# Kernel tuning notes

Hardware: AMD Instinct MI355X
Metric: run time of the kernel (lower is better)

The kernel has to match this reference:

```python
import jax, jax.numpy as jnp
import numpy as np

N_NODES, N_EDGES, WIDTH = 50000, 640000, 128


def setup_inputs() -> dict:
    key = jax.random.key(0)
    k1, k2, k3 = jax.random.split(key, 3)
    x = jax.random.normal(k1, (N_NODES, WIDTH), dtype=jnp.float32)
    e = jax.random.randint(k2, (2, N_EDGES), 0, N_NODES, dtype=jnp.int32)
    # LinearBlock(2*width, width): Linear(256 -> 128) + ReLU
    W = jax.random.normal(k3, (WIDTH, 2 * WIDTH), dtype=jnp.float32) * (1.0 / np.sqrt(2 * WIDTH))
    b = jnp.zeros((WIDTH,), dtype=jnp.float32)
    return {"x": x, "e": e, "W": W, "b": b}


def reference(x, e, W, b):
    src, dst = e[0], e[1]
    # gather-subtract: diffs[k] = x[dst_k] - x[src_k]  -> [E, width]
    diffs = x[dst] - x[src]
    n = x.shape[0]
    # scatter_max over destination nodes; torch_scatter leaves empty segments at 0
    maxes = jax.ops.segment_max(diffs, dst, num_segments=n)  # [N, width]
    deg = jax.ops.segment_sum(jnp.ones((dst.shape[0],), jnp.float32), dst, num_segments=n)
    maxes = jnp.where((deg > 0)[:, None], maxes, 0.0)
    # LinearBlock (Linear + ReLU) on concat, then residual
    h = jnp.concatenate([x, maxes], axis=1)  # [N, 2*width]
    return x + jax.nn.relu(h @ W.T + b)
```

## Files before the change

### kernel.cpp

```cpp
#include <hip/hip_runtime.h>
#include <hip/hip_bf16.h>

#define WIDTH   128
#define NNODES  50000
#define NEDGES  640000
#define NTILES  3125
#define WLDS_STRIDE 264

#define RBLK    32
#define SSEG    8
#define RSZ     1563
#define SEG_I4  20000
#define C0      16
#define CAPB    128

#define BIN_BLOCKS  (RBLK * SSEG)
#define CVT_BLOCKS  1563
#define GRID_PREP   (BIN_BLOCKS + CVT_BLOCKS + 1)

typedef __attribute__((ext_vector_type(8))) short  short8;
typedef __attribute__((ext_vector_type(4))) short  short4_t;
typedef __attribute__((ext_vector_type(4))) float  float4_t;

__device__ inline short f2bf(float f) {
    union { float f; unsigned int u; } a;
    a.f = f;
    unsigned int r = a.u + 0x7FFFu + ((a.u >> 16) & 1u);
    return (short)(r >> 16);
}
__device__ inline unsigned int pack2bf(float a, float b) {
    unsigned int lo = (unsigned short)f2bf(a);
    unsigned int hi = (unsigned short)f2bf(b);
    return lo | (hi << 16);
}
__device__ inline float bflo(unsigned int u) { return __uint_as_float(u << 16); }
__device__ inline float bfhi(unsigned int u) { return __uint_as_float(u & 0xFFFF0000u); }

__global__ __launch_bounds__(1024) void prep_kernel(
    const float* __restrict__ x, const int* __restrict__ e,
    const float* __restrict__ W,
    uint2* __restrict__ xb2, uint2* __restrict__ wb2,
    int* __restrict__ counts2, int* __restrict__ buckets)
{
    __shared__ int cnt[RSZ];
    const int bid = blockIdx.x;
    const int tid = threadIdx.x;

    if (bid < BIN_BLOCKS) {
        int r = bid & (RBLK - 1);
        int s = bid >> 5;
        int base = r * RSZ;
        int rsz  = NNODES - base; if (rsz > RSZ) rsz = RSZ;

        for (int i = tid; i < RSZ; i += 1024) cnt[i] = 0;
        __syncthreads();

        const int4* dst4 = (const int4*)(e + NEDGES + s * (SEG_I4 * 4));
        const int4* src4 = (const int4*)(e + s * (SEG_I4 * 4));

        int i = tid;
        int4 d = (i < SEG_I4) ? dst4[i] : make_int4(-1, -1, -1, -1);
        while (i < SEG_I4) {
            int inx = i + 1024;
            int4 dn = d;
            if (inx < SEG_I4) dn = dst4[inx];

            unsigned a0 = (unsigned)(d.x - base);
            unsigned a1 = (unsigned)(d.y - base);
            unsigned a2 = (unsigned)(d.z - base);
            unsigned a3 = (unsigned)(d.w - base);
            bool m0 = a0 < (unsigned)rsz;
            bool m1 = a1 < (unsigned)rsz;
            bool m2 = a2 < (unsigned)rsz;
            bool m3 = a3 < (unsigned)rsz;
            if (m0 | m1 | m2 | m3) {
                int4 sv = src4[i];
                if (m0) { int p = atomicAdd(&cnt[a0], 1); if (p < C0) buckets[d.x * CAPB + s * C0 + p] = sv.x; }
                if (m1) { int p = atomicAdd(&cnt[a1], 1); if (p < C0) buckets[d.y * CAPB + s * C0 + p] = sv.y; }
                if (m2) { int p = atomicAdd(&cnt[a2], 1); if (p < C0) buckets[d.z * CAPB + s * C0 + p] = sv.z; }
                if (m3) { int p = atomicAdd(&cnt[a3], 1); if (p < C0) buckets[d.w * CAPB + s * C0 + p] = sv.w; }
            }
            d = dn; i = inx;
        }
        __syncthreads();
        for (int i2 = tid; i2 < rsz; i2 += 1024) {
            int c = cnt[i2]; if (c > C0) c = C0;
            counts2[(base + i2) * SSEG + s] = c;
        }
    } else if (bid < BIN_BLOCKS + CVT_BLOCKS) {
        int i = (bid - BIN_BLOCKS) * 1024 + tid;
        if (i < 1600000) {
            float4 v = ((const float4*)x)[i];
            uint2 p; p.x = pack2bf(v.x, v.y); p.y = pack2bf(v.z, v.w);
            xb2[i] = p;
        }
    } else {
        for (int j = tid; j < 8192; j += 1024) {
            float4 v = ((const float4*)W)[j];
            uint2 p; p.x = pack2bf(v.x, v.y); p.y = pack2bf(v.z, v.w);
            wb2[j] = p;
        }
    }
}

__global__ __launch_bounds__(256) void gather_min_bf16_kernel(
    const uint2* __restrict__ xb2, const int* __restrict__ counts2,
    const int* __restrict__ buckets, uint2* __restrict__ maxes2)
{
    int wave = (blockIdx.x * 256 + threadIdx.x) >> 6;
    int lane = threadIdx.x & 63;
    if (wave >= NNODES) return;
    int node = wave;

    int s0 = lane >> 4;
    int j  = lane & 15;
    int c0 = counts2[node * SSEG + s0];
    int c1 = counts2[node * SSEG + 4 + s0];
    int idx0 = buckets[node * CAPB + lane];
    int idx1 = buckets[node * CAPB + 64 + lane];
    bool v0 = j < c0;
    bool v1 = j < c1;
    unsigned long long m0 = __ballot(v0);
    unsigned long long m1 = __ballot(v1);
    int p0 = __builtin_amdgcn_mbcnt_hi((unsigned)(m0 >> 32),
             __builtin_amdgcn_mbcnt_lo((unsigned)m0, 0));
    int popc0 = __popcll(m0);
    int p1 = popc0 + __builtin_amdgcn_mbcnt_hi((unsigned)(m1 >> 32),
                     __builtin_amdgcn_mbcnt_lo((unsigned)m1, 0));
    int deg = popc0 + __popcll(m1);
    int t0 = v0 ? p0 : 63;
    int t1 = v1 ? p1 : 63;
    int r0 = __builtin_amdgcn_ds_permute(t0 << 2, idx0);
    int r1 = __builtin_amdgcn_ds_permute(t1 << 2, idx1);
    int myidx = (lane < popc0) ? r0 : r1;

    int h  = lane >> 5;
    int cl = lane & 31;

    float4 m; m.x = 3.4e38f; m.y = 3.4e38f; m.z = 3.4e38f; m.w = 3.4e38f;
#pragma unroll 1
    for (int j0 = 0; j0 < deg; j0 += 16) {
        uint2 v[8];
#pragma unroll
        for (int u = 0; u < 8; ++u) {
            int jc = j0 + 2 * u + h;
            jc = jc < deg ? jc : deg - 1;
            int src = __shfl(myidx, jc);
            v[u] = xb2[(size_t)src * 32 + cl];
        }
#pragma unroll
        for (int u = 0; u < 8; ++u) {
            m.x = fminf(m.x, bflo(v[u].x));
            m.y = fminf(m.y, bfhi(v[u].x));
            m.z = fminf(m.z, bflo(v[u].y));
            m.w = fminf(m.w, bfhi(v[u].y));
        }
    }
    m.x = fminf(m.x, __shfl_xor(m.x, 32));
    m.y = fminf(m.y, __shfl_xor(m.y, 32));
    m.z = fminf(m.z, __shfl_xor(m.z, 32));
    m.w = fminf(m.w, __shfl_xor(m.w, 32));

    if (h == 0) {
        uint2 o;
        if (deg > 0) {
            uint2 xv = xb2[(size_t)node * 32 + cl];
            o.x = pack2bf(bflo(xv.x) - m.x, bfhi(xv.x) - m.y);
            o.y = pack2bf(bflo(xv.y) - m.z, bfhi(xv.y) - m.w);
        } else {
            o.x = 0u; o.y = 0u;
        }
        maxes2[(size_t)node * 32 + cl] = o;
    }
}

__global__ __launch_bounds__(256) void fill_kernel(
    const int* __restrict__ e, int* __restrict__ counts, int* __restrict__ buckets)
{
    int i = blockIdx.x * 256 + threadIdx.x;
    if (i >= NEDGES) return;
    int src = e[i];
    int dst = e[NEDGES + i];
    int pos = atomicAdd(&counts[dst], 1);
    if (pos < 64) buckets[dst * 64 + pos] = src;
}

__global__ __launch_bounds__(256) void gather_min_fp32_kernel(
    const float* __restrict__ x, const int* __restrict__ counts,
    const int* __restrict__ buckets, unsigned int* __restrict__ maxes_u32)
{
    int wave = (blockIdx.x * 256 + threadIdx.x) >> 6;
    int lane = threadIdx.x & 63;
    if (wave >= NNODES) return;
    int node = wave;
    int deg  = counts[node];
    deg = deg > 64 ? 64 : deg;

    int myidx = (lane < deg) ? buckets[node * 64 + lane] : 0;
    int c = lane * 2;
    float2 m; m.x = 3.4e38f; m.y = 3.4e38f;
#pragma unroll 1
    for (int j0 = 0; j0 < deg; j0 += 8) {
        float2 v[8];
#pragma unroll
        for (int u = 0; u < 8; ++u) {
            int jc = j0 + u;
            jc = jc < deg ? jc : deg - 1;
            int src = __shfl(myidx, jc);
            v[u] = *(const float2*)(x + (size_t)src * WIDTH + c);
        }
#pragma unroll
        for (int u = 0; u < 8; ++u) {
            m.x = fminf(m.x, v[u].x);
            m.y = fminf(m.y, v[u].y);
        }
    }
    float2 o;
    if (deg > 0) {
        float2 xv = *(const float2*)(x + (size_t)node * WIDTH + c);
        o.x = xv.x - m.x;
        o.y = xv.y - m.y;
    } else { o.x = 0.f; o.y = 0.f; }
    maxes_u32[(size_t)node * 64 + lane] = pack2bf(o.x, o.y);
}

template<bool FAST>
__global__ __launch_bounds__(256, 2) void fused_gemm_kernel(
    const float* __restrict__ x, const short* __restrict__ xb,
    const short* __restrict__ maxes,
    const float* __restrict__ W, const short* __restrict__ Wb,
    const float* __restrict__ b, float* __restrict__ out)
{
    __shared__ short Wlds[WIDTH * WLDS_STRIDE];

    const int t = threadIdx.x;

    if (FAST) {
#pragma unroll
        for (int i = 0; i < 32; ++i) {
            int idx8 = t + i * 256;
            int flat = idx8 << 3;
            short8 w = *(const short8*)(Wb + flat);
            int n = flat >> 8;
            int k = flat & 255;
            *(short4_t*)&Wlds[n * WLDS_STRIDE + k]     = *(short4_t*)&w;
            *(short4_t*)&Wlds[n * WLDS_STRIDE + k + 4] = *((short4_t*)&w + 1);
        }
    } else {
#pragma unroll
        for (int i = 0; i < 32; ++i) {
            int idx4 = t + i * 256;
            int flat = idx4 << 2;
            float4 w = *(const float4*)(W + flat);
            int n = flat >> 8;
            int k = flat & 255;
            short4_t s;
            s.x = f2bf(w.x); s.y = f2bf(w.y); s.z = f2bf(w.z); s.w = f2bf(w.w);
            *(short4_t*)&Wlds[n * WLDS_STRIDE + k] = s;
        }
    }
    __syncthreads();

    const int wave  = t >> 6;
    const int lane  = t & 63;
    const int lm    = lane & 15;
    const int quad  = lane >> 4;
    const int nhalf = wave & 1;
    const int wpair = wave >> 1;
    const int ncol_base = nhalf * 64;

    short8 bfrag[4][8];
#pragma unroll
    for (int nt = 0; nt < 4; ++nt) {
        int n = ncol_base + nt * 16 + lm;
#pragma unroll
        for (int kt = 0; kt < 8; ++kt) {
            int k = kt * 32 + quad * 8;
            bfrag[nt][kt] = *(const short8*)&Wlds[n * WLDS_STRIDE + k];
        }
    }

    const int stride = gridDim.x * 2;
#pragma unroll 1
    for (int tile = blockIdx.x * 2 + wpair; tile < NTILES; tile += stride) {
        int row = tile * 16 + lm;
        const float* xr  = x     + (size_t)row * WIDTH;
        const short* xbr = FAST ? (xb + (size_t)row * WIDTH) : nullptr;
        const short* mr  = maxes + (size_t)row * WIDTH;

        float4_t acc[4];
#pragma unroll
        for (int nt = 0; nt < 4; ++nt) { acc[nt].x = 0.f; acc[nt].y = 0.f; acc[nt].z = 0.f; acc[nt].w = 0.f; }

#pragma unroll
        for (int kt = 0; kt < 8; ++kt) {
            int k = kt * 32 + quad * 8;
            short8 afrag;
            if (k < WIDTH) {
                if (FAST) {
                    afrag = *(const short8*)(xbr + k);
                } else {
                    float4 v0 = *(const float4*)(xr + k);
                    float4 v1 = *(const float4*)(xr + k + 4);
                    afrag[0] = f2bf(v0.x); afrag[1] = f2bf(v0.y);
                    afrag[2] = f2bf(v0.z); afrag[3] = f2bf(v0.w);
                    afrag[4] = f2bf(v1.x); afrag[5] = f2bf(v1.y);
                    afrag[6] = f2bf(v1.z); afrag[7] = f2bf(v1.w);
                }
            } else {
                afrag = *(const short8*)(mr + (k - WIDTH));
            }
#pragma unroll
            for (int nt = 0; nt < 4; ++nt) {
                acc[nt] = __builtin_amdgcn_mfma_f32_16x16x32_bf16(
                    afrag, bfrag[nt][kt], acc[nt], 0, 0, 0);
            }
        }

#pragma unroll
        for (int nt = 0; nt < 4; ++nt) {
            int col = ncol_base + nt * 16 + lm;
            float bias = b[col];
#pragma unroll
            for (int r = 0; r < 4; ++r) {
                int orow = tile * 16 + quad * 4 + r;
                float v = acc[nt][r] + bias;
                v = v > 0.f ? v : 0.f;
                size_t off = (size_t)orow * WIDTH + col;
                out[off] = x[off] + v;
            }
        }
    }
}

extern "C" void kernel_launch(void* const* d_in, const int* in_sizes, int n_in,
                              void* d_out, int out_size, void* d_ws, size_t ws_size,
                              hipStream_t stream) {
    const float* x = (const float*)d_in[0];
    const int*   e = (const int*)  d_in[1];
    const float* W = (const float*)d_in[2];
    const float* b = (const float*)d_in[3];
    float* out = (float*)d_out;

    char* ws = (char*)d_ws;

    const size_t off_buckets = 1600512;
    const size_t off_maxes   = off_buckets + 25600000;
    const size_t off_xb      = off_maxes + 12800000;
    const size_t off_wb      = off_xb + 12800000;
    const size_t need        = off_wb + 65536;

    if (ws_size >= need) {
        int*          counts2 = (int*)ws;
        int*          buckets = (int*)(ws + off_buckets);
        unsigned int* maxes   = (unsigned int*)(ws + off_maxes);
        short*        xb      = (short*)(ws + off_xb);
        short*        wb      = (short*)(ws + off_wb);

        prep_kernel<<<GRID_PREP, 1024, 0, stream>>>(
            x, e, W, (uint2*)xb, (uint2*)wb, counts2, buckets);
        gather_min_bf16_kernel<<<(NNODES + 3) / 4, 256, 0, stream>>>(
            (const uint2*)xb, counts2, buckets, (uint2*)maxes);
        fused_gemm_kernel<true><<<512, 256, 0, stream>>>(
            x, xb, (const short*)maxes, W, wb, b, out);
    } else {
        int*          counts  = (int*)ws;
        int*          buckets = (int*)(ws + 262144);
        unsigned int* maxes   = (unsigned int*)(ws + 262144 + 12800000);

        hipMemsetAsync(counts, 0, 262144, stream);
        fill_kernel<<<(NEDGES + 255) / 256, 256, 0, stream>>>(e, counts, buckets);
        gather_min_fp32_kernel<<<(NNODES + 3) / 4, 256, 0, stream>>>(
            x, counts, buckets, maxes);
        fused_gemm_kernel<false><<<512, 256, 0, stream>>>(
            x, nullptr, (const short*)maxes, W, nullptr, b, out);
    }
}
```

Baseline: 144.0 us.

## Fuse neighbor min-gather into GEMM kernel via LDS staging of maxes

Merges the gather-min kernel into the GEMM kernel. Each block computes the aggregated maxes for 32 nodes into shared memory, then runs MFMA on them, and W fragments are held in registers instead of LDS. This removes the global round-trip of the maxes buffer and one kernel launch. The binning in prep also switches to 16 larger node ranges per segment, with fewer range-check blocks but more LDS counters. The risks are a heavier register footprint, since 32 short8 W fragments are kept per thread, and serialized gather/GEMM phases with syncthreads inside each block.

```diff
diff --git a/kernel.cpp b/kernel.cpp
--- a/kernel.cpp
+++ b/kernel.cpp
@@ -5,11 +5,11 @@
 #define NNODES  50000
 #define NEDGES  640000
 #define NTILES  3125
-#define WLDS_STRIDE 264
-
-#define RBLK    32
+#define NPAIRS  1563
+
+#define RBLK    16
 #define SSEG    8
-#define RSZ     1563
+#define RSZ     3125
 #define SEG_I4  20000
 #define C0      16
 #define CAPB    128
@@ -17,6 +17,8 @@
 #define BIN_BLOCKS  (RBLK * SSEG)
 #define CVT_BLOCKS  1563
 #define GRID_PREP   (BIN_BLOCKS + CVT_BLOCKS + 1)
+
+#define MSTRIDE 136
 
 typedef __attribute__((ext_vector_type(8))) short  short8;
 typedef __attribute__((ext_vector_type(4))) short  short4_t;
@@ -48,9 +50,8 @@
 
     if (bid < BIN_BLOCKS) {
         int r = bid & (RBLK - 1);
-        int s = bid >> 5;
+        int s = bid >> 4;
         int base = r * RSZ;
-        int rsz  = NNODES - base; if (rsz > RSZ) rsz = RSZ;
 
         for (int i = tid; i < RSZ; i += 1024) cnt[i] = 0;
         __syncthreads();
@@ -69,10 +70,10 @@
             unsigned a1 = (unsigned)(d.y - base);
             unsigned a2 = (unsigned)(d.z - base);
             unsigned a3 = (unsigned)(d.w - base);
-            bool m0 = a0 < (unsigned)rsz;
-            bool m1 = a1 < (unsigned)rsz;
-            bool m2 = a2 < (unsigned)rsz;
-            bool m3 = a3 < (unsigned)rsz;
+            bool m0 = a0 < (unsigned)RSZ;
+            bool m1 = a1 < (unsigned)RSZ;
+            bool m2 = a2 < (unsigned)RSZ;
+            bool m3 = a3 < (unsigned)RSZ;
             if (m0 | m1 | m2 | m3) {
                 int4 sv = src4[i];
                 if (m0) { int p = atomicAdd(&cnt[a0], 1); if (p < C0) buckets[d.x * CAPB + s * C0 + p] = sv.x; }
@@ -83,7 +84,7 @@
             d = dn; i = inx;
         }
         __syncthreads();
-        for (int i2 = tid; i2 < rsz; i2 += 1024) {
+        for (int i2 = tid; i2 < RSZ; i2 += 1024) {
             int c = cnt[i2]; if (c > C0) c = C0;
             counts2[(base + i2) * SSEG + s] = c;
         }
@@ -103,74 +104,148 @@
     }
 }
 
-__global__ __launch_bounds__(256) void gather_min_bf16_kernel(
-    const uint2* __restrict__ xb2, const int* __restrict__ counts2,
-    const int* __restrict__ buckets, uint2* __restrict__ maxes2)
+__global__ __launch_bounds__(256, 2) void gg_kernel(
+    const float* __restrict__ x, const short* __restrict__ xb,
+    const short* __restrict__ Wb, const float* __restrict__ b,
+    const int* __restrict__ counts2, const int* __restrict__ buckets,
+    float* __restrict__ out)
 {
-    int wave = (blockIdx.x * 256 + threadIdx.x) >> 6;
-    int lane = threadIdx.x & 63;
-    if (wave >= NNODES) return;
-    int node = wave;
-
-    int s0 = lane >> 4;
-    int j  = lane & 15;
-    int c0 = counts2[node * SSEG + s0];
-    int c1 = counts2[node * SSEG + 4 + s0];
-    int idx0 = buckets[node * CAPB + lane];
-    int idx1 = buckets[node * CAPB + 64 + lane];
-    bool v0 = j < c0;
-    bool v1 = j < c1;
-    unsigned long long m0 = __ballot(v0);
-    unsigned long long m1 = __ballot(v1);
-    int p0 = __builtin_amdgcn_mbcnt_hi((unsigned)(m0 >> 32),
-             __builtin_amdgcn_mbcnt_lo((unsigned)m0, 0));
-    int popc0 = __popcll(m0);
-    int p1 = popc0 + __builtin_amdgcn_mbcnt_hi((unsigned)(m1 >> 32),
-                     __builtin_amdgcn_mbcnt_lo((unsigned)m1, 0));
-    int deg = popc0 + __popcll(m1);
-    int t0 = v0 ? p0 : 63;
-    int t1 = v1 ? p1 : 63;
-    int r0 = __builtin_amdgcn_ds_permute(t0 << 2, idx0);
-    int r1 = __builtin_amdgcn_ds_permute(t1 << 2, idx1);
-    int myidx = (lane < popc0) ? r0 : r1;
-
-    int h  = lane >> 5;
-    int cl = lane & 31;
-
-    float4 m; m.x = 3.4e38f; m.y = 3.4e38f; m.z = 3.4e38f; m.w = 3.4e38f;
+    __shared__ short maxLDS[32 * MSTRIDE];
+
+    const int t     = threadIdx.x;
+    const int wave  = t >> 6;
+    const int lane  = t & 63;
+    const int lm    = lane & 15;
+    const int quad  = lane >> 4;
+    const int nhalf = wave & 1;
+    const int wpair = wave >> 1;
+    const int ncol_base = nhalf * 64;
+    const int h  = lane >> 5;
+    const int cl = lane & 31;
+
+    short8 bfrag[4][8];
+#pragma unroll
+    for (int nt = 0; nt < 4; ++nt) {
+        int n = ncol_base + nt * 16 + lm;
+#pragma unroll
+        for (int kt = 0; kt < 8; ++kt) {
+            int k = kt * 32 + quad * 8;
+            bfrag[nt][kt] = *(const short8*)(Wb + n * 256 + k);
+        }
+    }
+    float bias[4];
+#pragma unroll
+    for (int nt = 0; nt < 4; ++nt) bias[nt] = b[ncol_base + nt * 16 + lm];
+
 #pragma unroll 1
-    for (int j0 = 0; j0 < deg; j0 += 16) {
-        uint2 v[8];
-#pragma unroll
-        for (int u = 0; u < 8; ++u) {
-            int jc = j0 + 2 * u + h;
-            jc = jc < deg ? jc : deg - 1;
-            int src = __shfl(myidx, jc);
-            v[u] = xb2[(size_t)src * 32 + cl];
-        }
-#pragma unroll
-        for (int u = 0; u < 8; ++u) {
-            m.x = fminf(m.x, bflo(v[u].x));
-            m.y = fminf(m.y, bfhi(v[u].x));
-            m.z = fminf(m.z, bflo(v[u].y));
-            m.w = fminf(m.w, bfhi(v[u].y));
-        }
-    }
-    m.x = fminf(m.x, __shfl_xor(m.x, 32));
-    m.y = fminf(m.y, __shfl_xor(m.y, 32));
-    m.z = fminf(m.z, __shfl_xor(m.z, 32));
-    m.w = fminf(m.w, __shfl_xor(m.w, 32));
-
-    if (h == 0) {
-        uint2 o;
-        if (deg > 0) {
-            uint2 xv = xb2[(size_t)node * 32 + cl];
-            o.x = pack2bf(bflo(xv.x) - m.x, bfhi(xv.x) - m.y);
-            o.y = pack2bf(bflo(xv.y) - m.z, bfhi(xv.y) - m.w);
-        } else {
-            o.x = 0u; o.y = 0u;
-        }
-        maxes2[(size_t)node * 32 + cl] = o;
+    for (int p = blockIdx.x; p < NPAIRS; p += gridDim.x) {
+        int nbase = p * 32;
+
+#pragma unroll 1
+        for (int i = 0; i < 8; ++i) {
+            int ln   = wave * 8 + i;
+            int node = nbase + ln;
+            if (node < NNODES) {
+                int s0 = lane >> 4;
+                int j  = lane & 15;
+                int c0 = counts2[node * SSEG + s0];
+                int c1 = counts2[node * SSEG + 4 + s0];
+                int idx0 = buckets[node * CAPB + lane];
+                int idx1 = buckets[node * CAPB + 64 + lane];
+                bool v0 = j < c0;
+                bool v1 = j < c1;
+                unsigned long long m0 = __ballot(v0);
+                unsigned long long m1 = __ballot(v1);
+                int p0 = __builtin_amdgcn_mbcnt_hi((unsigned)(m0 >> 32),
+                         __builtin_amdgcn_mbcnt_lo((unsigned)m0, 0));
+                int popc0 = __popcll(m0);
+                int p1 = popc0 + __builtin_amdgcn_mbcnt_hi((unsigned)(m1 >> 32),
+                                 __builtin_amdgcn_mbcnt_lo((unsigned)m1, 0));
+                int deg = popc0 + __popcll(m1);
+                int t0 = v0 ? p0 : 63;
+                int t1 = v1 ? p1 : 63;
+                int r0 = __builtin_amdgcn_ds_permute(t0 << 2, idx0);
+                int r1 = __builtin_amdgcn_ds_permute(t1 << 2, idx1);
+                int myidx = (lane < popc0) ? r0 : r1;
+
+                float4 m; m.x = 3.4e38f; m.y = 3.4e38f; m.z = 3.4e38f; m.w = 3.4e38f;
+#pragma unroll 1
+                for (int j0 = 0; j0 < deg; j0 += 16) {
+                    uint2 v[8];
+#pragma unroll
+                    for (int u = 0; u < 8; ++u) {
+                        int jc = j0 + 2 * u + h;
+                        jc = jc < deg ? jc : deg - 1;
+                        int src = __shfl(myidx, jc);
+                        v[u] = *(const uint2*)(xb + (size_t)src * WIDTH + cl * 4);
+                    }
+#pragma unroll
+                    for (int u = 0; u < 8; ++u) {
+                        m.x = fminf(m.x, bflo(v[u].x));
+                        m.y = fminf(m.y, bfhi(v[u].x));
+                        m.z = fminf(m.z, bflo(v[u].y));
+                        m.w = fminf(m.w, bfhi(v[u].y));
+                    }
+                }
+                m.x = fminf(m.x, __shfl_xor(m.x, 32));
+                m.y = fminf(m.y, __shfl_xor(m.y, 32));
+                m.z = fminf(m.z, __shfl_xor(m.z, 32));
+                m.w = fminf(m.w, __shfl_xor(m.w, 32));
+
+                if (h == 0) {
+                    uint2 o;
+                    if (deg > 0) {
+                        uint2 xv = *(const uint2*)(xb + (size_t)node * WIDTH + cl * 4);
+                        o.x = pack2bf(bflo(xv.x) - m.x, bfhi(xv.x) - m.y);
+                        o.y = pack2bf(bflo(xv.y) - m.z, bfhi(xv.y) - m.w);
+                    } else {
+                        o.x = 0u; o.y = 0u;
+                    }
+                    *(uint2*)&maxLDS[ln * MSTRIDE + cl * 4] = o;
+                }
+            }
+        }
+        __syncthreads();
+
+        int tile = p * 2 + wpair;
+        if (tile < NTILES) {
+            int row = tile * 16 + lm;
+            const short* xbr = xb + (size_t)row * WIDTH;
+            const short* mls = &maxLDS[(wpair * 16 + lm) * MSTRIDE];
+
+            float4_t acc[4];
+#pragma unroll
+            for (int nt = 0; nt < 4; ++nt) { acc[nt].x = 0.f; acc[nt].y = 0.f; acc[nt].z = 0.f; acc[nt].w = 0.f; }
+
+#pragma unroll
+            for (int kt = 0; kt < 8; ++kt) {
+                short8 afrag;
+                if (kt < 4) {
+                    afrag = *(const short8*)(xbr + kt * 32 + quad * 8);
+                } else {
+                    afrag = *(const short8*)(mls + (kt - 4) * 32 + quad * 8);
+                }
+#pragma unroll
+                for (int nt = 0; nt < 4; ++nt) {
+                    acc[nt] = __builtin_amdgcn_mfma_f32_16x16x32_bf16(
+                        afrag, bfrag[nt][kt], acc[nt], 0, 0, 0);
+                }
+            }
+
+#pragma unroll
+            for (int nt = 0; nt < 4; ++nt) {
+                int col = ncol_base + nt * 16 + lm;
+#pragma unroll
+                for (int r = 0; r < 4; ++r) {
+                    int orow = tile * 16 + quad * 4 + r;
+                    float v = acc[nt][r] + bias[nt];
+                    v = v > 0.f ? v : 0.f;
+                    size_t off = (size_t)orow * WIDTH + col;
+                    out[off] = x[off] + v;
+                }
+            }
+        }
+        __syncthreads();
     }
 }
 
@@ -224,40 +299,24 @@
     maxes_u32[(size_t)node * 64 + lane] = pack2bf(o.x, o.y);
 }
 
-template<bool FAST>
-__global__ __launch_bounds__(256, 2) void fused_gemm_kernel(
-    const float* __restrict__ x, const short* __restrict__ xb,
-    const short* __restrict__ maxes,
-    const float* __restrict__ W, const short* __restrict__ Wb,
-    const float* __restrict__ b, float* __restrict__ out)
+#define WLDS_STRIDE 264
+__global__ __launch_bounds__(256, 2) void gemm_fallback_kernel(
+    const float* __restrict__ x, const short* __restrict__ maxes,
+    const float* __restrict__ W, const float* __restrict__ b,
+    float* __restrict__ out)
 {
     __shared__ short Wlds[WIDTH * WLDS_STRIDE];
-
     const int t = threadIdx.x;
-
-    if (FAST) {
-#pragma unroll
-        for (int i = 0; i < 32; ++i) {
-            int idx8 = t + i * 256;
-            int flat = idx8 << 3;
-            short8 w = *(const short8*)(Wb + flat);
-            int n = flat >> 8;
-            int k = flat & 255;
-            *(short4_t*)&Wlds[n * WLDS_STRIDE + k]     = *(short4_t*)&w;
-            *(short4_t*)&Wlds[n * WLDS_STRIDE + k + 4] = *((short4_t*)&w + 1);
-        }
-    } else {
-#pragma unroll
-        for (int i = 0; i < 32; ++i) {
-            int idx4 = t + i * 256;
-            int flat = idx4 << 2;
-            float4 w = *(const float4*)(W + flat);
-            int n = flat >> 8;
-            int k = flat & 255;
-            short4_t s;
-            s.x = f2bf(w.x); s.y = f2bf(w.y); s.z = f2bf(w.z); s.w = f2bf(w.w);
-            *(short4_t*)&Wlds[n * WLDS_STRIDE + k] = s;
-        }
+#pragma unroll
+    for (int i = 0; i < 32; ++i) {
+        int idx4 = t + i * 256;
+        int flat = idx4 << 2;
+        float4 w = *(const float4*)(W + flat);
+        int n = flat >> 8;
+        int k = flat & 255;
+        short4_t s;
+        s.x = f2bf(w.x); s.y = f2bf(w.y); s.z = f2bf(w.z); s.w = f2bf(w.w);
+        *(short4_t*)&Wlds[n * WLDS_STRIDE + k] = s;
     }
     __syncthreads();
 
@@ -284,9 +343,8 @@
 #pragma unroll 1
     for (int tile = blockIdx.x * 2 + wpair; tile < NTILES; tile += stride) {
         int row = tile * 16 + lm;
-        const float* xr  = x     + (size_t)row * WIDTH;
-        const short* xbr = FAST ? (xb + (size_t)row * WIDTH) : nullptr;
-        const short* mr  = maxes + (size_t)row * WIDTH;
+        const float* xr = x     + (size_t)row * WIDTH;
+        const short* mr = maxes + (size_t)row * WIDTH;
 
         float4_t acc[4];
 #pragma unroll
@@ -297,16 +355,12 @@
             int k = kt * 32 + quad * 8;
             short8 afrag;
             if (k < WIDTH) {
-                if (FAST) {
-                    afrag = *(const short8*)(xbr + k);
-                } else {
-                    float4 v0 = *(const float4*)(xr + k);
-                    float4 v1 = *(const float4*)(xr + k + 4);
-                    afrag[0] = f2bf(v0.x); afrag[1] = f2bf(v0.y);
-                    afrag[2] = f2bf(v0.z); afrag[3] = f2bf(v0.w);
-                    afrag[4] = f2bf(v1.x); afrag[5] = f2bf(v1.y);
-                    afrag[6] = f2bf(v1.z); afrag[7] = f2bf(v1.w);
-                }
+                float4 v0 = *(const float4*)(xr + k);
+                float4 v1 = *(const float4*)(xr + k + 4);
+                afrag[0] = f2bf(v0.x); afrag[1] = f2bf(v0.y);
+                afrag[2] = f2bf(v0.z); afrag[3] = f2bf(v0.w);
+                afrag[4] = f2bf(v1.x); afrag[5] = f2bf(v1.y);
+                afrag[6] = f2bf(v1.z); afrag[7] = f2bf(v1.w);
             } else {
                 afrag = *(const short8*)(mr + (k - WIDTH));
             }
@@ -345,24 +399,20 @@
     char* ws = (char*)d_ws;
 
     const size_t off_buckets = 1600512;
-    const size_t off_maxes   = off_buckets + 25600000;
-    const size_t off_xb      = off_maxes + 12800000;
+    const size_t off_xb      = off_buckets + 25600000;
     const size_t off_wb      = off_xb + 12800000;
     const size_t need        = off_wb + 65536;
 
     if (ws_size >= need) {
-        int*          counts2 = (int*)ws;
-        int*          buckets = (int*)(ws + off_buckets);
-        unsigned int* maxes   = (unsigned int*)(ws + off_maxes);
-        short*        xb      = (short*)(ws + off_xb);
-        short*        wb      = (short*)(ws + off_wb);
+        int*   counts2 = (int*)ws;
+        int*   buckets = (int*)(ws + off_buckets);
+        short* xb      = (short*)(ws + off_xb);
+        short* wb      = (short*)(ws + off_wb);
 
         prep_kernel<<<GRID_PREP, 1024, 0, stream>>>(
             x, e, W, (uint2*)xb, (uint2*)wb, counts2, buckets);
-        gather_min_bf16_kernel<<<(NNODES + 3) / 4, 256, 0, stream>>>(
-            (const uint2*)xb, counts2, buckets, (uint2*)maxes);
-        fused_gemm_kernel<true><<<512, 256, 0, stream>>>(
-            x, xb, (const short*)maxes, W, wb, b, out);
+        gg_kernel<<<512, 256, 0, stream>>>(
+            x, xb, wb, b, counts2, buckets, out);
     } else {
         int*          counts  = (int*)ws;
         int*          buckets = (int*)(ws + 262144);
@@ -372,7 +422,7 @@
         fill_kernel<<<(NEDGES + 255) / 256, 256, 0, stream>>>(e, counts, buckets);
         gather_min_fp32_kernel<<<(NNODES + 3) / 4, 256, 0, stream>>>(
             x, counts, buckets, maxes);
-        fused_gemm_kernel<false><<<512, 256, 0, stream>>>(
-            x, nullptr, (const short*)maxes, W, nullptr, b, out);
-    }
-}
+        gemm_fallback_kernel<<<512, 256, 0, stream>>>(
+            x, (const short*)maxes, W, b, out);
+    }
+}
```

Measured after the change: 170.1 us. +18.2%, slower.
